# Kernel tuning notes

Measured on AMD Instinct MI355X. Metric: run time of the kernel, lower is better.

## Reference

```python
import jax, jax.numpy as jnp
import numpy as np

N_NODES = 100000
N_EDGES = 1600000
NFEAT, NHID, NCLASS = 256, 256, 64
NLAYERS = 4


def _gcn_norm(edge_index, n_nodes):
    # PyG GCNConv default: add self-loops, symmetric normalization
    src, dst = edge_index[0], edge_index[1]
    loop = jnp.arange(n_nodes, dtype=edge_index.dtype)
    src = jnp.concatenate([src, loop])
    dst = jnp.concatenate([dst, loop])
    deg = jax.ops.segment_sum(jnp.ones_like(dst, dtype=jnp.float32), dst,
                              num_segments=n_nodes)
    dinv = jnp.where(deg > 0, jax.lax.rsqrt(deg), 0.0)
    norm = dinv[src] * dinv[dst]  # [E+N]
    return src, dst, norm


def _gcn_layer(X, W, b, src, dst, norm, n_nodes):
    H = X @ W                      # [N, out]
    msg = H[src] * norm[:, None]   # [E+N, out] gather + scale
    out = jax.ops.segment_sum(msg, dst, num_segments=n_nodes)
    return out + b


def setup_inputs() -> dict:
    key = jax.random.key(0)
    ks = jax.random.split(key, 8)
    x = jax.random.normal(ks[0], (N_NODES, NFEAT), dtype=jnp.float32)
    edge_index = jax.random.randint(ks[1], (2, N_EDGES), 0, N_NODES, dtype=jnp.int32)
    def glorot(k, fan_in, fan_out):
        s = jnp.sqrt(6.0 / (fan_in + fan_out))
        return jax.random.uniform(k, (fan_in, fan_out), jnp.float32, -s, s)
    return {
        "x": x,
        "W_enc": glorot(ks[2], NFEAT, NHID),
        "b_enc": jnp.zeros((NHID,), jnp.float32),
        "W_conv": glorot(ks[3], NHID, NHID),
        "b_conv": jnp.zeros((NHID,), jnp.float32),
        "W_dec": glorot(ks[4], NHID, NCLASS),
        "b_dec": jnp.zeros((NCLASS,), jnp.float32),
        "edge_index": edge_index,
    }


def reference(x, W_enc, b_enc, W_conv, b_conv, W_dec, b_dec, edge_index):
    n_nodes = x.shape[0]
    src, dst, norm = _gcn_norm(edge_index, n_nodes)
    # dropout probs are 0 (drop_in=drop=0) -> identity
    X = jax.nn.relu(_gcn_layer(x, W_enc, b_enc, src, dst, norm, n_nodes))
    for _ in range(NLAYERS):
        X = jax.nn.relu(_gcn_layer(X, W_conv, b_conv, src, dst, norm, n_nodes))
    X = jax.nn.relu(_gcn_layer(X, W_dec, b_dec, src, dst, norm, n_nodes))
    return X
```

## Files before the change

kernel.cpp:

```cpp
#include <hip/hip_runtime.h>

#define N_NODES 100000
#define N_EDGES 1600000
#define MPAD    100096
#define NB_SCAN ((N_NODES + 255) / 256)

using short8  = __attribute__((ext_vector_type(8))) short;
using ushort8 = __attribute__((ext_vector_type(8))) unsigned short;
using f32x4   = __attribute__((ext_vector_type(4))) float;

__device__ inline unsigned short f2bf(float f) {
    unsigned u = __float_as_uint(f);
    unsigned r = (u + 0x7fffu + ((u >> 16) & 1u)) >> 16;
    return (unsigned short)r;
}
__device__ inline float bf2f(unsigned short h) {
    return __uint_as_float(((unsigned)h) << 16);
}


__global__ __launch_bounds__(256) void k_init(int* __restrict__ indeg, int n) {
    int i = blockIdx.x * blockDim.x + threadIdx.x;
    if (i < n) indeg[i] = 0;
}

__global__ __launch_bounds__(256) void k_indeg(const int* __restrict__ dst,
                                               int* __restrict__ indeg, int e) {
    int i = blockIdx.x * blockDim.x + threadIdx.x;
    if (i < e) atomicAdd(&indeg[dst[i]], 1);
}

__global__ __launch_bounds__(256) void k_scan_blocks(const int* __restrict__ indeg,
                                                     int* __restrict__ blksum, int n) {
    int i = blockIdx.x * 256 + threadIdx.x;
    int v = (i < n) ? indeg[i] : 0;
#pragma unroll
    for (int o = 32; o > 0; o >>= 1) v += __shfl_down(v, o, 64);
    __shared__ int ws[4];
    if ((threadIdx.x & 63) == 0) ws[threadIdx.x >> 6] = v;
    __syncthreads();
    if (threadIdx.x == 0) blksum[blockIdx.x] = ws[0] + ws[1] + ws[2] + ws[3];
}

__global__ __launch_bounds__(512) void k_scan_top(const int* __restrict__ blksum,
                                                  int* __restrict__ blkpref,
                                                  int* __restrict__ offsets, int nb, int n) {
    __shared__ int s[512];
    int t = threadIdx.x;
    int v = (t < nb) ? blksum[t] : 0;
    s[t] = v;
    __syncthreads();
    for (int o = 1; o < 512; o <<= 1) {
        int u = (t >= o) ? s[t - o] : 0;
        __syncthreads();
        s[t] += u;
        __syncthreads();
    }
    if (t < nb) blkpref[t] = (t == 0) ? 0 : s[t - 1];
    if (t == nb - 1) offsets[n] = s[t];
}

__global__ __launch_bounds__(256) void k_scan_final(const int* __restrict__ indeg,
                                                    const int* __restrict__ blkpref,
                                                    int* __restrict__ offsets,
                                                    float* __restrict__ dinv, int n) {
    __shared__ int s[256];
    int t = threadIdx.x;
    int i = blockIdx.x * 256 + t;
    int v = (i < n) ? indeg[i] : 0;
    s[t] = v;
    __syncthreads();
    for (int o = 1; o < 256; o <<= 1) {
        int u = (t >= o) ? s[t - o] : 0;
        __syncthreads();
        s[t] += u;
        __syncthreads();
    }
    if (i < n) {
        offsets[i] = blkpref[blockIdx.x] + s[t] - v;
        dinv[i] = rsqrtf((float)(v + 1));
    }
}

__global__ __launch_bounds__(256) void k_scatter(const int* __restrict__ src,
                                                 const int* __restrict__ dst,
                                                 const int* __restrict__ offsets,
                                                 int* __restrict__ indeg,
                                                 int* __restrict__ csr_src, int e) {
    int i = blockIdx.x * blockDim.x + threadIdx.x;
    if (i < e) {
        int d = dst[i];
        int pos = offsets[d] + atomicSub(&indeg[d], 1) - 1;
        csr_src[pos] = src[i];
    }
}


__global__ __launch_bounds__(256) void k_cvt_x(const float* __restrict__ x,
                                               unsigned short* __restrict__ xb) {
    int i = blockIdx.x * blockDim.x + threadIdx.x;
    int row = i >> 6;
    ushort4 o;
    if (row < N_NODES) {
        float4 v = *(const float4*)(x + (size_t)i * 4);
        o.x = f2bf(v.x); o.y = f2bf(v.y); o.z = f2bf(v.z); o.w = f2bf(v.w);
    } else {
        o.x = o.y = o.z = o.w = 0;
    }
    *(ushort4*)(xb + (size_t)i * 4) = o;
}

__global__ __launch_bounds__(256) void k_prep_w(const float* __restrict__ W,
                                                unsigned short* __restrict__ Wt, int N) {
    int i = blockIdx.x * blockDim.x + threadIdx.x;
    if (i < 256 * N) {
        int r = i / N, c = i - r * N;
        Wt[(size_t)c * 256 + r] = f2bf(W[i]);
    }
}


template <int BN>
__global__ __launch_bounds__(256) void k_mfma_gemm(const unsigned short* __restrict__ A,
                                                   const unsigned short* __restrict__ Bt,
                                                   const float* __restrict__ dinv,
                                                   unsigned short* __restrict__ C,
                                                   int Ntot) {
    constexpr int K = 256, BK = 64;
    constexpr int NFR = BN / 32;
    __shared__ char ldsA[128 * 128];
    __shared__ char ldsB[BN * 128];
    const int tid  = threadIdx.x;
    const int lane = tid & 63;
    const int wid  = tid >> 6;
    const int wr   = wid >> 1, wc = wid & 1;
    const int row0 = blockIdx.x * 128;
    const int col0 = blockIdx.y * BN;
    const int l15  = lane & 15, lhi = lane >> 4;

    f32x4 acc[4][NFR];
#pragma unroll
    for (int m = 0; m < 4; ++m)
#pragma unroll
        for (int n = 0; n < NFR; ++n) acc[m][n] = {0.f, 0.f, 0.f, 0.f};

    for (int k0 = 0; k0 < K; k0 += BK) {
#pragma unroll
        for (int j = 0; j < 4; ++j) {
            int ci = j * 256 + tid;
            int r = ci >> 3;
            int cb = (ci & 7) ^ (r & 7);
            const char* src = (const char*)(A + (size_t)(row0 + r) * K + k0) + cb * 16;
            __builtin_amdgcn_global_load_lds((const __attribute__((address_space(1))) void*)src,
                                             (__attribute__((address_space(3))) void*)(ldsA + ci * 16),
                                             16, 0, 0);
        }
#pragma unroll
        for (int j = 0; j < BN / 32; ++j) {
            int ci = j * 256 + tid;
            int r = ci >> 3;
            int cb = (ci & 7) ^ (r & 7);
            const char* src = (const char*)(Bt + (size_t)(col0 + r) * K + k0) + cb * 16;
            __builtin_amdgcn_global_load_lds((const __attribute__((address_space(1))) void*)src,
                                             (__attribute__((address_space(3))) void*)(ldsB + ci * 16),
                                             16, 0, 0);
        }
        __syncthreads();
#pragma unroll
        for (int kk = 0; kk < 2; ++kk) {
            short8 af[4], bfr[NFR];
            int cb = kk * 4 + lhi;
#pragma unroll
            for (int m = 0; m < 4; ++m) {
                int r = wr * 64 + m * 16 + l15;
                af[m] = *(const short8*)(ldsA + r * 128 + ((cb ^ (r & 7)) << 4));
            }
#pragma unroll
            for (int n = 0; n < NFR; ++n) {
                int r = wc * (NFR * 16) + n * 16 + l15;
                bfr[n] = *(const short8*)(ldsB + r * 128 + ((cb ^ (r & 7)) << 4));
            }
#pragma unroll
            for (int m = 0; m < 4; ++m)
#pragma unroll
                for (int n = 0; n < NFR; ++n)
                    acc[m][n] = __builtin_amdgcn_mfma_f32_16x16x32_bf16(af[m], bfr[n],
                                                                        acc[m][n], 0, 0, 0);
        }
        __syncthreads();
    }
#pragma unroll
    for (int m = 0; m < 4; ++m) {
        int rbase = row0 + wr * 64 + m * 16 + lhi * 4;
        float sc[4];
#pragma unroll
        for (int q = 0; q < 4; ++q) {
            int grow = rbase + q;
            sc[q] = (grow < N_NODES) ? dinv[grow] : 0.f;
        }
#pragma unroll
        for (int n = 0; n < NFR; ++n) {
            int col = col0 + wc * (NFR * 16) + n * 16 + l15;
#pragma unroll
            for (int q = 0; q < 4; ++q)
                C[(size_t)(rbase + q) * Ntot + col] = f2bf(acc[m][n][q] * sc[q]);
        }
    }
}


__global__ __launch_bounds__(256) void k_agg256(const unsigned short* __restrict__ H,
                                                const int* __restrict__ offsets,
                                                const int* __restrict__ csr_src,
                                                const float* __restrict__ dinv,
                                                const float* __restrict__ bias,
                                                unsigned short* __restrict__ out, int n) {
    const int wid = __builtin_amdgcn_readfirstlane((blockIdx.x * blockDim.x + threadIdx.x) >> 6);
    if (wid >= n) return;
    const int lane = threadIdx.x & 63;
    const int half = lane >> 5;
    const unsigned coff = (unsigned)(lane & 31) * 16u;

    float acc[8] = {};
    const int beg = offsets[wid], end = offsets[wid + 1];
    int e = beg;

    for (; e + 7 < end; e += 8) {
        int sj[8];
#pragma unroll
        for (int j = 0; j < 8; ++j) sj[j] = csr_src[e + j];
        unsigned o0 = (unsigned)(half ? sj[1] : sj[0]) * 512u + coff;
        unsigned o1 = (unsigned)(half ? sj[3] : sj[2]) * 512u + coff;
        unsigned o2 = (unsigned)(half ? sj[5] : sj[4]) * 512u + coff;
        unsigned o3 = (unsigned)(half ? sj[7] : sj[6]) * 512u + coff;
        ushort8 v0 = *(const ushort8*)((const char*)H + o0);
        ushort8 v1 = *(const ushort8*)((const char*)H + o1);
        ushort8 v2 = *(const ushort8*)((const char*)H + o2);
        ushort8 v3 = *(const ushort8*)((const char*)H + o3);
#pragma unroll
        for (int j = 0; j < 8; ++j) acc[j] += bf2f(v0[j]);
#pragma unroll
        for (int j = 0; j < 8; ++j) acc[j] += bf2f(v1[j]);
#pragma unroll
        for (int j = 0; j < 8; ++j) acc[j] += bf2f(v2[j]);
#pragma unroll
        for (int j = 0; j < 8; ++j) acc[j] += bf2f(v3[j]);
    }
    for (; e + 1 < end; e += 2) {
        int s0 = csr_src[e], s1 = csr_src[e + 1];
        unsigned off = (unsigned)(half ? s1 : s0) * 512u + coff;
        ushort8 v = *(const ushort8*)((const char*)H + off);
#pragma unroll
        for (int j = 0; j < 8; ++j) acc[j] += bf2f(v[j]);
    }
    {
        int has_tail = (e < end);
        int sA = has_tail ? csr_src[e] : wid;
        float wB = has_tail ? 1.f : 0.f;
        unsigned off = (unsigned)(half ? wid : sA) * 512u + coff;
        float w = half ? wB : 1.f;
        ushort8 v = *(const ushort8*)((const char*)H + off);
#pragma unroll
        for (int j = 0; j < 8; ++j) acc[j] = fmaf(bf2f(v[j]), w, acc[j]);
    }

#pragma unroll
    for (int j = 0; j < 8; ++j) acc[j] += __shfl_xor(acc[j], 32);

    if (half == 0) {
        float dv = dinv[wid];
        const float* bp = bias + (lane & 31) * 8;
        float4 b0 = *(const float4*)bp;
        float4 b1 = *(const float4*)(bp + 4);
        ushort8 o;
        o[0] = f2bf(fmaxf(fmaf(acc[0], dv, b0.x), 0.f));
        o[1] = f2bf(fmaxf(fmaf(acc[1], dv, b0.y), 0.f));
        o[2] = f2bf(fmaxf(fmaf(acc[2], dv, b0.z), 0.f));
        o[3] = f2bf(fmaxf(fmaf(acc[3], dv, b0.w), 0.f));
        o[4] = f2bf(fmaxf(fmaf(acc[4], dv, b1.x), 0.f));
        o[5] = f2bf(fmaxf(fmaf(acc[5], dv, b1.y), 0.f));
        o[6] = f2bf(fmaxf(fmaf(acc[6], dv, b1.z), 0.f));
        o[7] = f2bf(fmaxf(fmaf(acc[7], dv, b1.w), 0.f));
        *(ushort8*)((char*)out + (unsigned)wid * 512u + coff) = o;
    }
}


__global__ __launch_bounds__(256) void k_agg64(const unsigned short* __restrict__ H,
                                               const int* __restrict__ offsets,
                                               const int* __restrict__ csr_src,
                                               const float* __restrict__ dinv,
                                               const float* __restrict__ bias,
                                               float* __restrict__ out, int n) {
    const int wid = __builtin_amdgcn_readfirstlane((blockIdx.x * blockDim.x + threadIdx.x) >> 6);
    if (wid >= n) return;
    const int lane = threadIdx.x & 63;
    const int q = lane >> 4;
    const unsigned coff = (unsigned)(lane & 15) * 8u;

    float acc[4] = {};
    const int beg = offsets[wid], end = offsets[wid + 1];
    int e = beg;

    for (; e + 3 < end; e += 4) {
        int s0 = csr_src[e], s1 = csr_src[e + 1], s2 = csr_src[e + 2], s3 = csr_src[e + 3];
        int srow = s0;
        if (q == 1) srow = s1;
        else if (q == 2) srow = s2;
        else if (q == 3) srow = s3;
        ushort4 v = *(const ushort4*)((const char*)H + (unsigned)srow * 128u + coff);
        acc[0] += bf2f(v.x); acc[1] += bf2f(v.y);
        acc[2] += bf2f(v.z); acc[3] += bf2f(v.w);
    }
    {
        int r = end - e;
        int srow = wid; float w = 0.f;
        if (q < r) { srow = csr_src[e + q]; w = 1.f; }
        else if (q == r) { srow = wid; w = 1.f; }
        ushort4 v = *(const ushort4*)((const char*)H + (unsigned)srow * 128u + coff);
        acc[0] = fmaf(bf2f(v.x), w, acc[0]);
        acc[1] = fmaf(bf2f(v.y), w, acc[1]);
        acc[2] = fmaf(bf2f(v.z), w, acc[2]);
        acc[3] = fmaf(bf2f(v.w), w, acc[3]);
    }
#pragma unroll
    for (int j = 0; j < 4; ++j) {
        acc[j] += __shfl_xor(acc[j], 16);
        acc[j] += __shfl_xor(acc[j], 32);
    }
    if (q == 0) {
        float dv = dinv[wid];
        float4 b = *(const float4*)(bias + (lane & 15) * 4);
        float4 o = make_float4(fmaxf(fmaf(acc[0], dv, b.x), 0.f),
                               fmaxf(fmaf(acc[1], dv, b.y), 0.f),
                               fmaxf(fmaf(acc[2], dv, b.z), 0.f),
                               fmaxf(fmaf(acc[3], dv, b.w), 0.f));
        *(float4*)((char*)out + (size_t)wid * 256u + coff * 2u) = o;
    }
}


extern "C" void kernel_launch(void* const* d_in, const int* in_sizes, int n_in,
                              void* d_out, int out_size, void* d_ws, size_t ws_size,
                              hipStream_t stream) {
    const float* x      = (const float*)d_in[0];
    const float* W_enc  = (const float*)d_in[1];
    const float* b_enc  = (const float*)d_in[2];
    const float* W_conv = (const float*)d_in[3];
    const float* b_conv = (const float*)d_in[4];
    const float* W_dec  = (const float*)d_in[5];
    const float* b_dec  = (const float*)d_in[6];
    const int*   ei     = (const int*)d_in[7];

    const int N = N_NODES;
    const int E = N_EDGES;
    const int* src = ei;
    const int* dst = ei + E;

    size_t off = 0;
    auto carve = [&](size_t bytes) -> void* {
        void* p = (char*)d_ws + off;
        off = (off + bytes + 255) & ~(size_t)255;
        return p;
    };
    unsigned short* Xb      = (unsigned short*)carve((size_t)MPAD * 256 * 2);
    unsigned short* Hb      = (unsigned short*)carve((size_t)MPAD * 256 * 2);
    unsigned short* Wt_enc  = (unsigned short*)carve((size_t)256 * 256 * 2);
    unsigned short* Wt_conv = (unsigned short*)carve((size_t)256 * 256 * 2);
    unsigned short* Wt_dec  = (unsigned short*)carve((size_t)64 * 256 * 2);
    int*            indeg   = (int*)carve((size_t)N * sizeof(int));
    float*          dinv    = (float*)carve((size_t)N * sizeof(float));
    int*            offsets = (int*)carve((size_t)(N + 1) * sizeof(int));
    int*            csr_src = (int*)carve((size_t)E * sizeof(int));
    int*            blksum  = (int*)carve((size_t)NB_SCAN * sizeof(int));
    int*            blkpref = (int*)carve((size_t)NB_SCAN * sizeof(int));
    (void)ws_size;

    k_cvt_x<<<MPAD / 4, 256, 0, stream>>>(x, Xb);
    k_prep_w<<<(256 * 256 + 255) / 256, 256, 0, stream>>>(W_enc, Wt_enc, 256);
    k_prep_w<<<(256 * 256 + 255) / 256, 256, 0, stream>>>(W_conv, Wt_conv, 256);
    k_prep_w<<<(256 * 64 + 255) / 256, 256, 0, stream>>>(W_dec, Wt_dec, 64);
    k_init<<<(N + 255) / 256, 256, 0, stream>>>(indeg, N);
    k_indeg<<<(E + 255) / 256, 256, 0, stream>>>(dst, indeg, E);
    k_scan_blocks<<<NB_SCAN, 256, 0, stream>>>(indeg, blksum, N);
    k_scan_top<<<1, 512, 0, stream>>>(blksum, blkpref, offsets, NB_SCAN, N);
    k_scan_final<<<NB_SCAN, 256, 0, stream>>>(indeg, blkpref, offsets, dinv, N);
    k_scatter<<<(E + 255) / 256, 256, 0, stream>>>(src, dst, offsets, indeg, csr_src, E);

    dim3 gconv(MPAD / 128, 2);
    dim3 gdec(MPAD / 128, 1);
    const int agg_blocks = (N + 3) / 4;

    k_mfma_gemm<128><<<gconv, 256, 0, stream>>>(Xb, Wt_enc, dinv, Hb, 256);
    k_agg256<<<agg_blocks, 256, 0, stream>>>(Hb, offsets, csr_src, dinv, b_enc, Xb, N);
    for (int l = 0; l < 4; ++l) {
        k_mfma_gemm<128><<<gconv, 256, 0, stream>>>(Xb, Wt_conv, dinv, Hb, 256);
        k_agg256<<<agg_blocks, 256, 0, stream>>>(Hb, offsets, csr_src, dinv, b_conv, Xb, N);
    }
    k_mfma_gemm<64><<<gdec, 256, 0, stream>>>(Xb, Wt_dec, dinv, Hb, 64);
    k_agg64<<<agg_blocks, 256, 0, stream>>>(Hb, offsets, csr_src, dinv, b_dec,
                                            (float*)d_out, N);
}
```

Baseline: 1.027 ms.

## Build CSR via two-pass source-then-destination counting sort for sorted neighbor lists

Result: slower. 1.201 ms (+17.0%).

```diff
diff --git a/kernel.cpp b/kernel.cpp
--- a/kernel.cpp
+++ b/kernel.cpp
@@ -19,21 +19,31 @@
 }
 
 
-__global__ __launch_bounds__(256) void k_init(int* __restrict__ indeg, int n) {
+__global__ __launch_bounds__(256) void k_init(int* __restrict__ scnt,
+                                              int* __restrict__ dcnt, int n) {
     int i = blockIdx.x * blockDim.x + threadIdx.x;
-    if (i < n) indeg[i] = 0;
-}
-
-__global__ __launch_bounds__(256) void k_indeg(const int* __restrict__ dst,
-                                               int* __restrict__ indeg, int e) {
-    int i = blockIdx.x * blockDim.x + threadIdx.x;
-    if (i < e) atomicAdd(&indeg[dst[i]], 1);
-}
-
-__global__ __launch_bounds__(256) void k_scan_blocks(const int* __restrict__ indeg,
+    if (i < n) { scnt[i] = 0; dcnt[i] = 0; }
+}
+
+__global__ __launch_bounds__(256) void k_hist(const int* __restrict__ src,
+                                              const int* __restrict__ dst,
+                                              int* __restrict__ scnt,
+                                              int* __restrict__ dcnt, int e) {
+    int i = (blockIdx.x * blockDim.x + threadIdx.x) * 4;
+    if (i < e) {
+        int4 s = *(const int4*)(src + i);
+        int4 d = *(const int4*)(dst + i);
+        atomicAdd(&scnt[s.x], 1); atomicAdd(&scnt[s.y], 1);
+        atomicAdd(&scnt[s.z], 1); atomicAdd(&scnt[s.w], 1);
+        atomicAdd(&dcnt[d.x], 1); atomicAdd(&dcnt[d.y], 1);
+        atomicAdd(&dcnt[d.z], 1); atomicAdd(&dcnt[d.w], 1);
+    }
+}
+
+__global__ __launch_bounds__(256) void k_scan_blocks(const int* __restrict__ cnt,
                                                      int* __restrict__ blksum, int n) {
     int i = blockIdx.x * 256 + threadIdx.x;
-    int v = (i < n) ? indeg[i] : 0;
+    int v = (i < n) ? cnt[i] : 0;
 #pragma unroll
     for (int o = 32; o > 0; o >>= 1) v += __shfl_down(v, o, 64);
     __shared__ int ws[4];
@@ -60,14 +70,14 @@
     if (t == nb - 1) offsets[n] = s[t];
 }
 
-__global__ __launch_bounds__(256) void k_scan_final(const int* __restrict__ indeg,
+__global__ __launch_bounds__(256) void k_scan_final(const int* __restrict__ cnt,
                                                     const int* __restrict__ blkpref,
                                                     int* __restrict__ offsets,
                                                     float* __restrict__ dinv, int n) {
     __shared__ int s[256];
     int t = threadIdx.x;
     int i = blockIdx.x * 256 + t;
-    int v = (i < n) ? indeg[i] : 0;
+    int v = (i < n) ? cnt[i] : 0;
     s[t] = v;
     __syncthreads();
     for (int o = 1; o < 256; o <<= 1) {
@@ -78,20 +88,32 @@
     }
     if (i < n) {
         offsets[i] = blkpref[blockIdx.x] + s[t] - v;
-        dinv[i] = rsqrtf((float)(v + 1));
-    }
-}
-
-__global__ __launch_bounds__(256) void k_scatter(const int* __restrict__ src,
-                                                 const int* __restrict__ dst,
-                                                 const int* __restrict__ offsets,
-                                                 int* __restrict__ indeg,
-                                                 int* __restrict__ csr_src, int e) {
+        if (dinv) dinv[i] = rsqrtf((float)(v + 1));
+    }
+}
+
+__global__ __launch_bounds__(256) void k_scatter1(const int* __restrict__ src,
+                                                  const int* __restrict__ dst,
+                                                  const int* __restrict__ soff,
+                                                  int* __restrict__ scnt,
+                                                  int2* __restrict__ tmp, int e) {
     int i = blockIdx.x * blockDim.x + threadIdx.x;
     if (i < e) {
-        int d = dst[i];
-        int pos = offsets[d] + atomicSub(&indeg[d], 1) - 1;
-        csr_src[pos] = src[i];
+        int s = src[i];
+        int p = soff[s] + atomicSub(&scnt[s], 1) - 1;
+        tmp[p] = make_int2(s, dst[i]);
+    }
+}
+
+__global__ __launch_bounds__(256) void k_scatter2(const int2* __restrict__ tmp,
+                                                  const int* __restrict__ doff,
+                                                  int* __restrict__ dcnt,
+                                                  int* __restrict__ csr_src, int e) {
+    int p = blockIdx.x * blockDim.x + threadIdx.x;
+    if (p < e) {
+        int2 sd = tmp[p];
+        int pos = doff[sd.y] + atomicSub(&dcnt[sd.y], 1) - 1;
+        csr_src[pos] = sd.x;
     }
 }
 
@@ -120,7 +142,7 @@
 }
 
 
-template <int BN>
+template <int BN, bool DSCALE>
 __global__ __launch_bounds__(256) void k_mfma_gemm(const unsigned short* __restrict__ A,
                                                    const unsigned short* __restrict__ Bt,
                                                    const float* __restrict__ dinv,
@@ -196,7 +218,7 @@
 #pragma unroll
         for (int q = 0; q < 4; ++q) {
             int grow = rbase + q;
-            sc[q] = (grow < N_NODES) ? dinv[grow] : 0.f;
+            sc[q] = DSCALE ? ((grow < N_NODES) ? dinv[grow] : 0.f) : 1.f;
         }
 #pragma unroll
         for (int n = 0; n < NFR; ++n) {
@@ -314,14 +336,14 @@
     }
     {
         int r = end - e;
-        int srow = wid; float w = 0.f;
-        if (q < r) { srow = csr_src[e + q]; w = 1.f; }
-        else if (q == r) { srow = wid; w = 1.f; }
+        int srow = wid; float wgt = 0.f;
+        if (q < r) { srow = csr_src[e + q]; wgt = 1.f; }
+        else if (q == r) { srow = wid; wgt = 1.f; }
         ushort4 v = *(const ushort4*)((const char*)H + (unsigned)srow * 128u + coff);
-        acc[0] = fmaf(bf2f(v.x), w, acc[0]);
-        acc[1] = fmaf(bf2f(v.y), w, acc[1]);
-        acc[2] = fmaf(bf2f(v.z), w, acc[2]);
-        acc[3] = fmaf(bf2f(v.w), w, acc[3]);
+        acc[0] = fmaf(bf2f(v.x), wgt, acc[0]);
+        acc[1] = fmaf(bf2f(v.y), wgt, acc[1]);
+        acc[2] = fmaf(bf2f(v.z), wgt, acc[2]);
+        acc[3] = fmaf(bf2f(v.w), wgt, acc[3]);
     }
 #pragma unroll
     for (int j = 0; j < 4; ++j) {
@@ -368,10 +390,13 @@
     unsigned short* Wt_enc  = (unsigned short*)carve((size_t)256 * 256 * 2);
     unsigned short* Wt_conv = (unsigned short*)carve((size_t)256 * 256 * 2);
     unsigned short* Wt_dec  = (unsigned short*)carve((size_t)64 * 256 * 2);
-    int*            indeg   = (int*)carve((size_t)N * sizeof(int));
+    int*            scnt    = (int*)carve((size_t)N * sizeof(int));
+    int*            dcnt    = (int*)carve((size_t)N * sizeof(int));
     float*          dinv    = (float*)carve((size_t)N * sizeof(float));
-    int*            offsets = (int*)carve((size_t)(N + 1) * sizeof(int));
+    int*            soff    = (int*)carve((size_t)(N + 1) * sizeof(int));
+    int*            doff    = (int*)carve((size_t)(N + 1) * sizeof(int));
     int*            csr_src = (int*)carve((size_t)E * sizeof(int));
+    int2*           tmp     = (int2*)carve((size_t)E * sizeof(int2));
     int*            blksum  = (int*)carve((size_t)NB_SCAN * sizeof(int));
     int*            blkpref = (int*)carve((size_t)NB_SCAN * sizeof(int));
     (void)ws_size;
@@ -380,24 +405,29 @@
     k_prep_w<<<(256 * 256 + 255) / 256, 256, 0, stream>>>(W_enc, Wt_enc, 256);
     k_prep_w<<<(256 * 256 + 255) / 256, 256, 0, stream>>>(W_conv, Wt_conv, 256);
     k_prep_w<<<(256 * 64 + 255) / 256, 256, 0, stream>>>(W_dec, Wt_dec, 64);
-    k_init<<<(N + 255) / 256, 256, 0, stream>>>(indeg, N);
-    k_indeg<<<(E + 255) / 256, 256, 0, stream>>>(dst, indeg, E);
-    k_scan_blocks<<<NB_SCAN, 256, 0, stream>>>(indeg, blksum, N);
-    k_scan_top<<<1, 512, 0, stream>>>(blksum, blkpref, offsets, NB_SCAN, N);
-    k_scan_final<<<NB_SCAN, 256, 0, stream>>>(indeg, blkpref, offsets, dinv, N);
-    k_scatter<<<(E + 255) / 256, 256, 0, stream>>>(src, dst, offsets, indeg, csr_src, E);
+
+    k_init<<<(N + 255) / 256, 256, 0, stream>>>(scnt, dcnt, N);
+    k_hist<<<(E / 4 + 255) / 256, 256, 0, stream>>>(src, dst, scnt, dcnt, E);
+    k_scan_blocks<<<NB_SCAN, 256, 0, stream>>>(scnt, blksum, N);
+    k_scan_top<<<1, 512, 0, stream>>>(blksum, blkpref, soff, NB_SCAN, N);
+    k_scan_final<<<NB_SCAN, 256, 0, stream>>>(scnt, blkpref, soff, nullptr, N);
+    k_scan_blocks<<<NB_SCAN, 256, 0, stream>>>(dcnt, blksum, N);
+    k_scan_top<<<1, 512, 0, stream>>>(blksum, blkpref, doff, NB_SCAN, N);
+    k_scan_final<<<NB_SCAN, 256, 0, stream>>>(dcnt, blkpref, doff, dinv, N);
+    k_scatter1<<<(E + 255) / 256, 256, 0, stream>>>(src, dst, soff, scnt, tmp, E);
+    k_scatter2<<<(E + 255) / 256, 256, 0, stream>>>(tmp, doff, dcnt, csr_src, E);
 
     dim3 gconv(MPAD / 128, 2);
     dim3 gdec(MPAD / 128, 1);
     const int agg_blocks = (N + 3) / 4;
 
-    k_mfma_gemm<128><<<gconv, 256, 0, stream>>>(Xb, Wt_enc, dinv, Hb, 256);
-    k_agg256<<<agg_blocks, 256, 0, stream>>>(Hb, offsets, csr_src, dinv, b_enc, Xb, N);
+    k_mfma_gemm<128, true><<<gconv, 256, 0, stream>>>(Xb, Wt_enc, dinv, Hb, 256);
+    k_agg256<<<agg_blocks, 256, 0, stream>>>(Hb, doff, csr_src, dinv, b_enc, Xb, N);
     for (int l = 0; l < 4; ++l) {
-        k_mfma_gemm<128><<<gconv, 256, 0, stream>>>(Xb, Wt_conv, dinv, Hb, 256);
-        k_agg256<<<agg_blocks, 256, 0, stream>>>(Hb, offsets, csr_src, dinv, b_conv, Xb, N);
-    }
-    k_mfma_gemm<64><<<gdec, 256, 0, stream>>>(Xb, Wt_dec, dinv, Hb, 64);
-    k_agg64<<<agg_blocks, 256, 0, stream>>>(Hb, offsets, csr_src, dinv, b_dec,
+        k_mfma_gemm<128, true><<<gconv, 256, 0, stream>>>(Xb, Wt_conv, dinv, Hb, 256);
+        k_agg256<<<agg_blocks, 256, 0, stream>>>(Hb, doff, csr_src, dinv, b_conv, Xb, N);
+    }
+    k_mfma_gemm<64, true><<<gdec, 256, 0, stream>>>(Xb, Wt_dec, dinv, Hb, 64);
+    k_agg64<<<agg_blocks, 256, 0, stream>>>(Hb, doff, csr_src, dinv, b_dec,
                                             (float*)d_out, N);
 }
```
